# Optimization experiments

Hardware: AMD Instinct MI355X
Metric: run time of the kernel (lower is better)

## Reference

```python
import jax, jax.numpy as jnp
import numpy as np

B, T, F, H = 512, 1024, 64, 512  # batch, timesteps, n_features, hidden_dims


def _lstm_cell(x, h, c, W_ih, W_hh, b_ih, b_hh):
    # torch.nn.LSTMCell gate order: i, f, g, o
    g = x @ W_ih.T + b_ih + h @ W_hh.T + b_hh
    i, f, gg, o = jnp.split(g, 4, axis=-1)
    c_new = jax.nn.sigmoid(f) * c + jax.nn.sigmoid(i) * jnp.tanh(gg)
    h_new = jax.nn.sigmoid(o) * jnp.tanh(c_new)
    return h_new, c_new


def setup_inputs() -> dict:
    key = jax.random.key(0)
    ks = jax.random.split(key, 9)
    s1 = 1.0 / np.sqrt(H)  # torch LSTMCell init scale for lstm1
    s2 = 1.0 / np.sqrt(F)  # for lstm2 (hidden size = n_features)
    u = lambda k, shape, s: jax.random.uniform(k, shape, jnp.float32, -s, s)
    return {
        "data": jax.random.normal(ks[0], (B, T * F), jnp.float32),
        "W_ih1": u(ks[1], (4 * H, F), s1),
        "W_hh1": u(ks[2], (4 * H, H), s1),
        "b_ih1": u(ks[3], (4 * H,), s1),
        "b_hh1": u(ks[4], (4 * H,), s1),
        "W_ih2": u(ks[5], (4 * F, H), s2),
        "W_hh2": u(ks[6], (4 * F, F), s2),
        "b_ih2": u(ks[7], (4 * F,), s2),
        "b_hh2": u(ks[8], (4 * F,), s2),
        "future": 0,
    }


def reference(data, W_ih1, W_hh1, b_ih1, b_hh1, W_ih2, W_hh2, b_ih2, b_hh2, future):
    x = data.reshape(B, T, F).transpose(1, 0, 2)  # [T, B, F] for scan
    h1 = jnp.zeros((B, H), data.dtype)
    c1 = jnp.zeros((B, H), data.dtype)
    h2 = jnp.zeros((B, F), data.dtype)
    c2 = jnp.zeros((B, F), data.dtype)  # this is the 'output' in the torch code

    def step(carry, x_t):
        h1, c1, h2, c2 = carry
        h1, c1 = _lstm_cell(x_t, h1, c1, W_ih1, W_hh1, b_ih1, b_hh1)
        # NOTE: original feeds c_t (cell state of lstm1) into lstm2, and the
        # per-step 'output' is lstm2's CELL state c2 (h_t2, output = lstm2(...)).
        h2, c2 = _lstm_cell(c1, h2, c2, W_ih2, W_hh2, b_ih2, b_hh2)
        return (h1, c1, h2, c2), c2

    (h1, c1, h2, c2), outs = jax.lax.scan(step, (h1, c1, h2, c2), x)
    outputs = [outs]  # [T, B, F]
    out_t = c2
    for _ in range(int(future)):  # future is a Python int constant
        h1, c1 = _lstm_cell(out_t, h1, c1, W_ih1, W_hh1, b_ih1, b_hh1)
        h2, out_t = _lstm_cell(c1, h2, out_t, W_ih2, W_hh2, b_ih2, b_hh2)
        outputs.append(out_t[None])
    out = jnp.concatenate(outputs, axis=0).transpose(1, 0, 2)  # [B, T+future, F]
    return jnp.squeeze(out, axis=2) if out.shape[2] == 1 else out
```

## Files before the change

### kernel.cpp

```cpp
#include <hip/hip_runtime.h>

#define Bn   512
#define Tn   1024
#define Fn   64
#define Hn   512
#define NGRP 16
#define GMEM 9
#define NBLK (NGRP * GMEM)
#define TRIES (1L << 22)

typedef short bf16x8 __attribute__((ext_vector_type(8)));
typedef float f32x4  __attribute__((ext_vector_type(4)));

__device__ __forceinline__ short f2bf(float f) {
    union { float f; unsigned u; } v; v.f = f;
    unsigned r = (v.u + 0x7FFFu + ((v.u >> 16) & 1u)) >> 16;
    return (short)(unsigned short)r;
}
__device__ __forceinline__ float sigm(float x) { return 1.f / (1.f + __expf(-x)); }
__device__ __forceinline__ float tanh_(float x) { return 2.f / (1.f + __expf(-2.f * x)) - 1.f; }

__device__ __forceinline__ bf16x8 cvt8(const float* p) {
    const float4 v0 = *(const float4*)p;
    const float4 v1 = *(const float4*)(p + 4);
    bf16x8 a;
    a[0] = f2bf(v0.x); a[1] = f2bf(v0.y); a[2] = f2bf(v0.z); a[3] = f2bf(v0.w);
    a[4] = f2bf(v1.x); a[5] = f2bf(v1.y); a[6] = f2bf(v1.z); a[7] = f2bf(v1.w);
    return a;
}

__device__ __forceinline__ void ldx16(bf16x8& d, const short* p) {
    asm volatile("global_load_dwordx4 %0, %1, off sc0 sc1" : "=v"(d) : "v"(p));
}
__device__ __forceinline__ void stx16(short* p, bf16x8 v) {
    asm volatile("global_store_dwordx4 %0, %1, off sc0 sc1" :: "v"(p), "v"(v) : "memory");
}
#define VMWAIT(N) do { \
    asm volatile("s_waitcnt vmcnt(" #N ")" ::: "memory"); \
    __builtin_amdgcn_sched_barrier(0); } while (0)

__device__ __forceinline__ int aldi(const int* p) {
    return __hip_atomic_load(p, __ATOMIC_RELAXED, __HIP_MEMORY_SCOPE_AGENT);
}

__device__ __forceinline__ void flag_arrive(int* slot, int val) {
    asm volatile("s_waitcnt vmcnt(0)" ::: "memory");
    __builtin_amdgcn_sched_barrier(0);
    __syncthreads();
    if (threadIdx.x == 0)
        __hip_atomic_store(slot, val, __ATOMIC_RELEASE, __HIP_MEMORY_SCOPE_AGENT);
}
__device__ __forceinline__ void flag_wait(const int* flags, int tgtA, int tgtB) {
    const int lane = threadIdx.x & 63;
    const int tgt = (lane < 8) ? tgtA : tgtB;
    long spins = 0;
    for (;;) {
        bool ok = (lane >= GMEM) || (aldi(flags + lane) >= tgt);
        if (__all(ok)) break;
        if (++spins > TRIES) break;
        __builtin_amdgcn_s_sleep(1);
    }
    __atomic_signal_fence(__ATOMIC_ACQUIRE);
    __builtin_amdgcn_sched_barrier(0);
}

__global__ void prep_kernel(const float* __restrict__ Wih1, const float* __restrict__ Whh1,
                            const float* __restrict__ Wih2, const float* __restrict__ Whh2,
                            const float* __restrict__ bih1, const float* __restrict__ bhh1,
                            const float* __restrict__ bih2, const float* __restrict__ bhh2,
                            short* __restrict__ h1g, short* __restrict__ h2g,
                            short* __restrict__ w1f, short* __restrict__ w2f,
                            float* __restrict__ bs1, float* __restrict__ bs2,
                            int* __restrict__ bar) {
    const int i0 = blockIdx.x * blockDim.x + threadIdx.x;
    const int stride = gridDim.x * blockDim.x;
    for (int i = i0; i < 1024; i += stride) bar[i] = 0;
    for (int i = i0; i < 2 * Bn * Hn; i += stride) h1g[i] = 0;
    for (int i = i0; i < 2 * Bn * Fn; i += stride) h2g[i] = 0;
    for (int i = i0; i < 2048 * 576; i += stride) {
        int kk = i & 31, n = (i >> 5) & 15, ct = (i >> 9) & 3;
        int r = i >> 11; int kb = r % 18; int ut = r / 18;
        int gcol = ct * 512 + ut * 16 + n;
        int k = kb * 32 + kk;
        float v = (k < 64) ? Wih1[gcol * 64 + k] : Whh1[gcol * 512 + (k - 64)];
        w1f[i] = f2bf(v);
    }
    for (int i = i0; i < 256 * 576; i += stride) {
        int kk = i & 31, n = (i >> 5) & 15, ct = (i >> 9) & 3;
        int r = i >> 11; int kb = r % 18; int ut4 = r / 18;
        int gcol = ct * 64 + ut4 * 16 + n;
        int k = kb * 32 + kk;
        float v = (k < 512) ? Wih2[gcol * 512 + k] : Whh2[gcol * 64 + (k - 512)];
        w2f[i] = f2bf(v);
    }
    for (int i = i0; i < 2048; i += stride) bs1[i] = bih1[i] + bhh1[i];
    for (int i = i0; i < 256;  i += stride) bs2[i] = bih2[i] + bhh2[i];
}

__global__ __launch_bounds__(256, 1) void lstm_kernel(
    const float* __restrict__ data,
    const short* __restrict__ w1f, const float* __restrict__ bs1,
    const short* __restrict__ w2f, const float* __restrict__ bs2,
    short* __restrict__ h1g, short* __restrict__ c1g,
    float* __restrict__ out, int* __restrict__ bar) {
    extern __shared__ short smem[];
    const int tid = threadIdx.x;
    const int lane = tid & 63, wv = tid >> 6;
    const int n = lane & 15, q = lane >> 4;
    const int wvc = wv;
    const int bid = blockIdx.x;
    const int rt = bid / GMEM, role = bid % GMEM;
    const f32x4 Z4 = {0.f, 0.f, 0.f, 0.f};
    const int rowbase = rt * 32;
    int* grp = bar + rt * 32;
    short* tile0 = smem + 16384;
    short* tile1 = smem + 18432;
    const int r0 = rowbase + n, r1 = rowbase + 16 + n;
    const int lr0 = n, lr1 = n + 16, sw = n & 7;

    if (role < 8) {
        const int ut = role * 4 + wvc;
        const int ucol = ut * 16 + n;
        const float bi_ = bs1[ucol], bf_ = bs1[512 + ucol], bg_ = bs1[1024 + ucol], bo_ = bs1[1536 + ucol];
        const short* wbase = w1f + ut * 36864 + n * 32 + q * 8;

        bf16x8 wr[16][4];
#pragma unroll
        for (int kb = 0; kb < 16; ++kb)
#pragma unroll
            for (int g = 0; g < 4; ++g)
                wr[kb][g] = *(const bf16x8*)(wbase + ((kb + 2) * 4 + g) * 512);

        f32x4 c1f[2]; c1f[0] = Z4; c1f[1] = Z4;

        for (int t = 0; t < Tn; ++t) {
            const short* h1r = h1g + (t & 1) * (Bn * Hn);
            short* h1w = h1g + ((t + 1) & 1) * (Bn * Hn);
            short* c1w = c1g + (t & 1) * (Bn * Hn);
            f32x4 acc[2][4];
#pragma unroll
            for (int a = 0; a < 2; ++a)
#pragma unroll
                for (int g = 0; g < 4; ++g) acc[a][g] = Z4;

            const float* x0 = data + (size_t)r0 * 65536 + t * 64;
            const float* x1 = data + (size_t)r1 * 65536 + t * 64;
#pragma unroll
            for (int kb = 0; kb < 2; ++kb) {
                const bf16x8 a0 = cvt8(x0 + kb * 32 + q * 8);
                const bf16x8 a1 = cvt8(x1 + kb * 32 + q * 8);
#pragma unroll
                for (int g = 0; g < 4; ++g) {
                    const bf16x8 b = *(const bf16x8*)(wbase + (kb * 4 + g) * 512);
                    acc[0][g] = __builtin_amdgcn_mfma_f32_16x16x32_bf16(a0, b, acc[0][g], 0, 0, 0);
                    acc[1][g] = __builtin_amdgcn_mfma_f32_16x16x32_bf16(a1, b, acc[1][g], 0, 0, 0);
                }
            }

            flag_wait(grp, t, t - 1);

            const short* gsrc = h1r + (size_t)rt * 16384;
            bf16x8 st[8];
            __builtin_amdgcn_sched_barrier(0);
#pragma unroll
            for (int i = 0; i < 8; ++i) ldx16(st[i], gsrc + (i * 256 + tid) * 8);
            VMWAIT(4);
#pragma unroll
            for (int i = 0; i < 4; ++i) {
                const int c = i * 256 + tid; const int row = c >> 6, col = c & 63;
                *(bf16x8*)&smem[row * 512 + ((col ^ (row & 7)) * 8)] = st[i];
            }
            VMWAIT(0);
#pragma unroll
            for (int i = 4; i < 8; ++i) {
                const int c = i * 256 + tid; const int row = c >> 6, col = c & 63;
                *(bf16x8*)&smem[row * 512 + ((col ^ (row & 7)) * 8)] = st[i];
            }
            __syncthreads();

#pragma unroll
            for (int kb = 0; kb < 16; ++kb) {
                const bf16x8 a0 = *(const bf16x8*)&smem[lr0 * 512 + (((kb * 4 + q) ^ sw) * 8)];
                const bf16x8 a1 = *(const bf16x8*)&smem[lr1 * 512 + (((kb * 4 + q) ^ sw) * 8)];
#pragma unroll
                for (int g = 0; g < 4; ++g) {
                    acc[0][g] = __builtin_amdgcn_mfma_f32_16x16x32_bf16(a0, wr[kb][g], acc[0][g], 0, 0, 0);
                    acc[1][g] = __builtin_amdgcn_mfma_f32_16x16x32_bf16(a1, wr[kb][g], acc[1][g], 0, 0, 0);
                }
            }

#pragma unroll
            for (int rt16 = 0; rt16 < 2; ++rt16) {
#pragma unroll
                for (int r = 0; r < 4; ++r) {
                    const float xi = acc[rt16][0][r] + bi_;
                    const float xf = acc[rt16][1][r] + bf_;
                    const float xg = acc[rt16][2][r] + bg_;
                    const float xo = acc[rt16][3][r] + bo_;
                    const float ii = sigm(xi), ff = sigm(xf), gg = tanh_(xg), oo = sigm(xo);
                    const float c = ff * c1f[rt16][r] + ii * gg;
                    c1f[rt16][r] = c;
                    const float h = oo * tanh_(c);
                    const int lr = rt16 * 16 + q * 4 + r;
                    const int lu = wvc * 16 + n;
                    tile0[lr * 64 + lu] = f2bf(h);
                    tile1[lr * 64 + lu] = f2bf(c);
                }
            }
            __syncthreads();
            {
                const int row = tid >> 3, part = tid & 7;
                const bf16x8 hv = *(const bf16x8*)&tile0[row * 64 + part * 8];
                const bf16x8 cv = *(const bf16x8*)&tile1[row * 64 + part * 8];
                short* gdst = h1w + (size_t)(rowbase + row) * 512 + role * 64 + part * 8;
                short* gdc  = c1w + (size_t)(rowbase + row) * 512 + role * 64 + part * 8;
                stx16(gdst, hv);
                stx16(gdc, cv);
            }
            flag_arrive(grp + role, t + 1);
        }
    } else {
        const int ut4 = wvc;
        const int ucol = ut4 * 16 + n;
        const float bi_ = bs2[ucol], bf_ = bs2[64 + ucol], bg_ = bs2[128 + ucol], bo_ = bs2[192 + ucol];
        const short* wbase = w2f + ut4 * 36864 + n * 32 + q * 8;

        bf16x8 wr[16][4];
#pragma unroll
        for (int kb = 0; kb < 16; ++kb)
#pragma unroll
            for (int g = 0; g < 4; ++g)
                wr[kb][g] = *(const bf16x8*)(wbase + (kb * 4 + g) * 512);
        bf16x8 wh[2][4];
#pragma unroll
        for (int kb2 = 0; kb2 < 2; ++kb2)
#pragma unroll
            for (int g = 0; g < 4; ++g)
                wh[kb2][g] = *(const bf16x8*)(wbase + ((16 + kb2) * 4 + g) * 512);

        for (int i = tid; i < 2048; i += 256) { tile0[i] = 0; tile1[i] = 0; }
        __syncthreads();

        f32x4 c2f[2]; c2f[0] = Z4; c2f[1] = Z4;

        for (int t = 0; t < Tn; ++t) {
            flag_wait(grp, t + 1, t);
            const short* c1r = c1g + (t & 1) * (Bn * Hn);
            const short* h2rd = (t & 1) ? tile1 : tile0;
            short* h2wr = (t & 1) ? tile0 : tile1;
            f32x4 acc[2][4];
#pragma unroll
            for (int a = 0; a < 2; ++a)
#pragma unroll
                for (int g = 0; g < 4; ++g) acc[a][g] = Z4;

            const short* gsrc = c1r + (size_t)rt * 16384;
            bf16x8 st[8];
            __builtin_amdgcn_sched_barrier(0);
#pragma unroll
            for (int i = 0; i < 8; ++i) ldx16(st[i], gsrc + (i * 256 + tid) * 8);
            VMWAIT(4);
#pragma unroll
            for (int i = 0; i < 4; ++i) {
                const int c = i * 256 + tid; const int row = c >> 6, col = c & 63;
                *(bf16x8*)&smem[row * 512 + ((col ^ (row & 7)) * 8)] = st[i];
            }
            VMWAIT(0);
#pragma unroll
            for (int i = 4; i < 8; ++i) {
                const int c = i * 256 + tid; const int row = c >> 6, col = c & 63;
                *(bf16x8*)&smem[row * 512 + ((col ^ (row & 7)) * 8)] = st[i];
            }
            __syncthreads();

#pragma unroll
            for (int kb = 0; kb < 16; ++kb) {
                const bf16x8 a0 = *(const bf16x8*)&smem[lr0 * 512 + (((kb * 4 + q) ^ sw) * 8)];
                const bf16x8 a1 = *(const bf16x8*)&smem[lr1 * 512 + (((kb * 4 + q) ^ sw) * 8)];
#pragma unroll
                for (int g = 0; g < 4; ++g) {
                    acc[0][g] = __builtin_amdgcn_mfma_f32_16x16x32_bf16(a0, wr[kb][g], acc[0][g], 0, 0, 0);
                    acc[1][g] = __builtin_amdgcn_mfma_f32_16x16x32_bf16(a1, wr[kb][g], acc[1][g], 0, 0, 0);
                }
            }
#pragma unroll
            for (int kb2 = 0; kb2 < 2; ++kb2) {
                const bf16x8 a0 = *(const bf16x8*)&h2rd[lr0 * 64 + (((kb2 * 4 + q) ^ sw) * 8)];
                const bf16x8 a1 = *(const bf16x8*)&h2rd[lr1 * 64 + (((kb2 * 4 + q) ^ sw) * 8)];
#pragma unroll
                for (int g = 0; g < 4; ++g) {
                    acc[0][g] = __builtin_amdgcn_mfma_f32_16x16x32_bf16(a0, wh[kb2][g], acc[0][g], 0, 0, 0);
                    acc[1][g] = __builtin_amdgcn_mfma_f32_16x16x32_bf16(a1, wh[kb2][g], acc[1][g], 0, 0, 0);
                }
            }

#pragma unroll
            for (int rt16 = 0; rt16 < 2; ++rt16) {
#pragma unroll
                for (int r = 0; r < 4; ++r) {
                    const float xi = acc[rt16][0][r] + bi_;
                    const float xf = acc[rt16][1][r] + bf_;
                    const float xg = acc[rt16][2][r] + bg_;
                    const float xo = acc[rt16][3][r] + bo_;
                    const float ii = sigm(xi), ff = sigm(xf), gg = tanh_(xg), oo = sigm(xo);
                    const float c = ff * c2f[rt16][r] + ii * gg;
                    c2f[rt16][r] = c;
                    const float h = oo * tanh_(c);
                    const int lr = rt16 * 16 + q * 4 + r;
                    const int lu = wvc * 16 + n;
                    out[(size_t)(rowbase + lr) * 65536 + (size_t)t * 64 + ucol] = c;
                    h2wr[lr * 64 + (((lu >> 3) ^ (lr & 7)) * 8) + (lu & 7)] = f2bf(h);
                }
            }
            flag_arrive(grp + 8, t + 1);
        }
    }
}

extern "C" void kernel_launch(void* const* d_in, const int* in_sizes, int n_in,
                              void* d_out, int out_size, void* d_ws, size_t ws_size,
                              hipStream_t stream) {
    const float* data = (const float*)d_in[0];
    const float* Wih1 = (const float*)d_in[1];
    const float* Whh1 = (const float*)d_in[2];
    const float* bih1 = (const float*)d_in[3];
    const float* bhh1 = (const float*)d_in[4];
    const float* Wih2 = (const float*)d_in[5];
    const float* Whh2 = (const float*)d_in[6];
    const float* bih2 = (const float*)d_in[7];
    const float* bhh2 = (const float*)d_in[8];
    float* out = (float*)d_out;

    char* w = (char*)d_ws;
    short* h1g = (short*)(w + 0);
    short* c1g = (short*)(w + 1048576);
    short* h2g = (short*)(w + 2097152);
    short* w2f = (short*)(w + 2228224);
    short* w1f = (short*)(w + 2523136);
    float* bs1 = (float*)(w + 4882432);
    float* bs2 = (float*)(w + 4890624);
    int* bar  = (int*)(w + 4891648);

    hipLaunchKernelGGL(prep_kernel, dim3(1024), dim3(256), 0, stream,
                       Wih1, Whh1, Wih2, Whh2, bih1, bhh1, bih2, bhh2,
                       h1g, h2g, w1f, w2f, bs1, bs2, bar);

    hipLaunchKernelGGL(lstm_kernel, dim3(NBLK), dim3(256), 40960, stream,
                       data, w1f, bs1, w2f, bs2, h1g, c1g, out, bar);
}
```

Before: 7.511 ms.

## Triple-buffer c1 handoff, reuse own h1 slice locally, pad LDS rows

The c1 exchange buffer becomes triple-buffered, so layer-1 blocks only wait for layer-2 to be two steps behind instead of one, which loosens coupling between the two stages. Each layer-1 block now loads only the seven foreign 64-column slices of h1 from global memory and takes its own slice from the local LDS tile written in the previous step, saving one global load per thread per step. LDS row strides are padded (516 and 68) and the tile writes are swizzled to reduce bank conflicts. The h1 store flag is raised before the c1 store, and a final arrive is added after the loop. This adds more workspace and more complex synchronisation logic.

```diff
diff --git a/kernel.cpp b/kernel.cpp
--- a/kernel.cpp
+++ b/kernel.cpp
@@ -8,6 +8,8 @@
 #define GMEM 9
 #define NBLK (NGRP * GMEM)
 #define TRIES (1L << 22)
+#define SLD  516
+#define TLD  68
 
 typedef short bf16x8 __attribute__((ext_vector_type(8)));
 typedef float f32x4  __attribute__((ext_vector_type(4)));
@@ -68,7 +70,7 @@
                             const float* __restrict__ Wih2, const float* __restrict__ Whh2,
                             const float* __restrict__ bih1, const float* __restrict__ bhh1,
                             const float* __restrict__ bih2, const float* __restrict__ bhh2,
-                            short* __restrict__ h1g, short* __restrict__ h2g,
+                            short* __restrict__ h1g, short* __restrict__ c1g,
                             short* __restrict__ w1f, short* __restrict__ w2f,
                             float* __restrict__ bs1, float* __restrict__ bs2,
                             int* __restrict__ bar) {
@@ -76,7 +78,7 @@
     const int stride = gridDim.x * blockDim.x;
     for (int i = i0; i < 1024; i += stride) bar[i] = 0;
     for (int i = i0; i < 2 * Bn * Hn; i += stride) h1g[i] = 0;
-    for (int i = i0; i < 2 * Bn * Fn; i += stride) h2g[i] = 0;
+    for (int i = i0; i < 3 * Bn * Hn; i += stride) c1g[i] = 0;
     for (int i = i0; i < 2048 * 576; i += stride) {
         int kk = i & 31, n = (i >> 5) & 15, ct = (i >> 9) & 3;
         int r = i >> 11; int kb = r % 18; int ut = r / 18;
@@ -113,10 +115,11 @@
     const f32x4 Z4 = {0.f, 0.f, 0.f, 0.f};
     const int rowbase = rt * 32;
     int* grp = bar + rt * 32;
-    short* tile0 = smem + 16384;
-    short* tile1 = smem + 18432;
+    short* tile0 = smem + 32 * SLD;
+    short* tile1 = tile0 + 32 * TLD;
     const int r0 = rowbase + n, r1 = rowbase + 16 + n;
     const int lr0 = n, lr1 = n + 16, sw = n & 7;
+    const int srow = tid >> 3, sd8 = tid & 7;
 
     if (role < 8) {
         const int ut = role * 4 + wvc;
@@ -131,12 +134,15 @@
             for (int g = 0; g < 4; ++g)
                 wr[kb][g] = *(const bf16x8*)(wbase + ((kb + 2) * 4 + g) * 512);
 
+        for (int i = tid; i < 32 * TLD; i += 256) tile0[i] = 0;
+        __syncthreads();
+
         f32x4 c1f[2]; c1f[0] = Z4; c1f[1] = Z4;
 
         for (int t = 0; t < Tn; ++t) {
             const short* h1r = h1g + (t & 1) * (Bn * Hn);
             short* h1w = h1g + ((t + 1) & 1) * (Bn * Hn);
-            short* c1w = c1g + (t & 1) * (Bn * Hn);
+            short* c1w = c1g + (t % 3) * (Bn * Hn);
             f32x4 acc[2][4];
 #pragma unroll
             for (int a = 0; a < 2; ++a)
@@ -156,32 +162,47 @@
                     acc[1][g] = __builtin_amdgcn_mfma_f32_16x16x32_bf16(a1, b, acc[1][g], 0, 0, 0);
                 }
             }
-
-            flag_wait(grp, t, t - 1);
-
-            const short* gsrc = h1r + (size_t)rt * 16384;
-            bf16x8 st[8];
+            bf16x8 aOwn[2][2];
+#pragma unroll
+            for (int kl = 0; kl < 2; ++kl) {
+                aOwn[kl][0] = *(const bf16x8*)&tile0[lr0 * TLD + ((((kl * 4 + q)) ^ sw) * 8)];
+                aOwn[kl][1] = *(const bf16x8*)&tile0[lr1 * TLD + ((((kl * 4 + q)) ^ sw) * 8)];
+            }
+
+            flag_wait(grp, t, t - 2);
+
+            const short* gsrc = h1r + (size_t)rowbase * 512;
+            bf16x8 st[7];
             __builtin_amdgcn_sched_barrier(0);
 #pragma unroll
-            for (int i = 0; i < 8; ++i) ldx16(st[i], gsrc + (i * 256 + tid) * 8);
-            VMWAIT(4);
+            for (int i = 0; i < 7; ++i) {
+                const int p = (role + 1 + i) & 7;
+                ldx16(st[i], gsrc + srow * 512 + p * 64 + sd8 * 8);
+            }
+            VMWAIT(3);
 #pragma unroll
             for (int i = 0; i < 4; ++i) {
-                const int c = i * 256 + tid; const int row = c >> 6, col = c & 63;
-                *(bf16x8*)&smem[row * 512 + ((col ^ (row & 7)) * 8)] = st[i];
+                const int p = (role + 1 + i) & 7;
+                *(bf16x8*)&smem[srow * SLD + ((p * 8 + (sd8 ^ (srow & 7))) * 8)] = st[i];
             }
             VMWAIT(0);
 #pragma unroll
-            for (int i = 4; i < 8; ++i) {
-                const int c = i * 256 + tid; const int row = c >> 6, col = c & 63;
-                *(bf16x8*)&smem[row * 512 + ((col ^ (row & 7)) * 8)] = st[i];
+            for (int i = 4; i < 7; ++i) {
+                const int p = (role + 1 + i) & 7;
+                *(bf16x8*)&smem[srow * SLD + ((p * 8 + (sd8 ^ (srow & 7))) * 8)] = st[i];
             }
             __syncthreads();
 
 #pragma unroll
             for (int kb = 0; kb < 16; ++kb) {
-                const bf16x8 a0 = *(const bf16x8*)&smem[lr0 * 512 + (((kb * 4 + q) ^ sw) * 8)];
-                const bf16x8 a1 = *(const bf16x8*)&smem[lr1 * 512 + (((kb * 4 + q) ^ sw) * 8)];
+                bf16x8 a0, a1;
+                if ((kb >> 1) == role) {
+                    a0 = aOwn[kb & 1][0];
+                    a1 = aOwn[kb & 1][1];
+                } else {
+                    a0 = *(const bf16x8*)&smem[lr0 * SLD + (((kb * 4 + q) ^ sw) * 8)];
+                    a1 = *(const bf16x8*)&smem[lr1 * SLD + (((kb * 4 + q) ^ sw) * 8)];
+                }
 #pragma unroll
                 for (int g = 0; g < 4; ++g) {
                     acc[0][g] = __builtin_amdgcn_mfma_f32_16x16x32_bf16(a0, wr[kb][g], acc[0][g], 0, 0, 0);
@@ -203,22 +224,25 @@
                     const float h = oo * tanh_(c);
                     const int lr = rt16 * 16 + q * 4 + r;
                     const int lu = wvc * 16 + n;
-                    tile0[lr * 64 + lu] = f2bf(h);
-                    tile1[lr * 64 + lu] = f2bf(c);
+                    const int slot = ((lu >> 3) ^ (lr & 7)) * 8 + (lu & 7);
+                    tile0[lr * TLD + slot] = f2bf(h);
+                    tile1[lr * TLD + slot] = f2bf(c);
                 }
             }
             __syncthreads();
             {
                 const int row = tid >> 3, part = tid & 7;
-                const bf16x8 hv = *(const bf16x8*)&tile0[row * 64 + part * 8];
-                const bf16x8 cv = *(const bf16x8*)&tile1[row * 64 + part * 8];
+                const int slot = (part ^ (row & 7)) * 8;
+                const bf16x8 hv = *(const bf16x8*)&tile0[row * TLD + slot];
+                const bf16x8 cv = *(const bf16x8*)&tile1[row * TLD + slot];
                 short* gdst = h1w + (size_t)(rowbase + row) * 512 + role * 64 + part * 8;
                 short* gdc  = c1w + (size_t)(rowbase + row) * 512 + role * 64 + part * 8;
                 stx16(gdst, hv);
+                flag_arrive(grp + role, t + 1);
                 stx16(gdc, cv);
             }
-            flag_arrive(grp + role, t + 1);
         }
+        flag_arrive(grp + role, Tn + 1);
     } else {
         const int ut4 = wvc;
         const int ucol = ut4 * 16 + n;
@@ -238,14 +262,14 @@
             for (int g = 0; g < 4; ++g)
                 wh[kb2][g] = *(const bf16x8*)(wbase + ((16 + kb2) * 4 + g) * 512);
 
-        for (int i = tid; i < 2048; i += 256) { tile0[i] = 0; tile1[i] = 0; }
+        for (int i = tid; i < 64 * TLD; i += 256) tile0[i] = 0;
         __syncthreads();
 
         f32x4 c2f[2]; c2f[0] = Z4; c2f[1] = Z4;
 
         for (int t = 0; t < Tn; ++t) {
-            flag_wait(grp, t + 1, t);
-            const short* c1r = c1g + (t & 1) * (Bn * Hn);
+            flag_wait(grp, t + 2, t);
+            const short* c1r = c1g + (t % 3) * (Bn * Hn);
             const short* h2rd = (t & 1) ? tile1 : tile0;
             short* h2wr = (t & 1) ? tile0 : tile1;
             f32x4 acc[2][4];
@@ -254,7 +278,7 @@
 #pragma unroll
                 for (int g = 0; g < 4; ++g) acc[a][g] = Z4;
 
-            const short* gsrc = c1r + (size_t)rt * 16384;
+            const short* gsrc = c1r + (size_t)rowbase * 512;
             bf16x8 st[8];
             __builtin_amdgcn_sched_barrier(0);
 #pragma unroll
@@ -262,21 +286,21 @@
             VMWAIT(4);
 #pragma unroll
             for (int i = 0; i < 4; ++i) {
-                const int c = i * 256 + tid; const int row = c >> 6, col = c & 63;
-                *(bf16x8*)&smem[row * 512 + ((col ^ (row & 7)) * 8)] = st[i];
+                const int row = i * 4 + wv; const int col = lane;
+                *(bf16x8*)&smem[row * SLD + ((col >> 3) * 8 + ((col & 7) ^ (row & 7))) * 8] = st[i];
             }
             VMWAIT(0);
 #pragma unroll
             for (int i = 4; i < 8; ++i) {
-                const int c = i * 256 + tid; const int row = c >> 6, col = c & 63;
-                *(bf16x8*)&smem[row * 512 + ((col ^ (row & 7)) * 8)] = st[i];
+                const int row = i * 4 + wv; const int col = lane;
+                *(bf16x8*)&smem[row * SLD + ((col >> 3) * 8 + ((col & 7) ^ (row & 7))) * 8] = st[i];
             }
             __syncthreads();
 
 #pragma unroll
             for (int kb = 0; kb < 16; ++kb) {
-                const bf16x8 a0 = *(const bf16x8*)&smem[lr0 * 512 + (((kb * 4 + q) ^ sw) * 8)];
-                const bf16x8 a1 = *(const bf16x8*)&smem[lr1 * 512 + (((kb * 4 + q) ^ sw) * 8)];
+                const bf16x8 a0 = *(const bf16x8*)&smem[lr0 * SLD + (((kb * 4 + q) ^ sw) * 8)];
+                const bf16x8 a1 = *(const bf16x8*)&smem[lr1 * SLD + (((kb * 4 + q) ^ sw) * 8)];
 #pragma unroll
                 for (int g = 0; g < 4; ++g) {
                     acc[0][g] = __builtin_amdgcn_mfma_f32_16x16x32_bf16(a0, wr[kb][g], acc[0][g], 0, 0, 0);
@@ -285,8 +309,8 @@
             }
 #pragma unroll
             for (int kb2 = 0; kb2 < 2; ++kb2) {
-                const bf16x8 a0 = *(const bf16x8*)&h2rd[lr0 * 64 + (((kb2 * 4 + q) ^ sw) * 8)];
-                const bf16x8 a1 = *(const bf16x8*)&h2rd[lr1 * 64 + (((kb2 * 4 + q) ^ sw) * 8)];
+                const bf16x8 a0 = *(const bf16x8*)&h2rd[lr0 * TLD + (((kb2 * 4 + q) ^ sw) * 8)];
+                const bf16x8 a1 = *(const bf16x8*)&h2rd[lr1 * TLD + (((kb2 * 4 + q) ^ sw) * 8)];
 #pragma unroll
                 for (int g = 0; g < 4; ++g) {
                     acc[0][g] = __builtin_amdgcn_mfma_f32_16x16x32_bf16(a0, wh[kb2][g], acc[0][g], 0, 0, 0);
@@ -309,7 +333,7 @@
                     const int lr = rt16 * 16 + q * 4 + r;
                     const int lu = wvc * 16 + n;
                     out[(size_t)(rowbase + lr) * 65536 + (size_t)t * 64 + ucol] = c;
-                    h2wr[lr * 64 + (((lu >> 3) ^ (lr & 7)) * 8) + (lu & 7)] = f2bf(h);
+                    h2wr[lr * TLD + ((lu >> 3) ^ (lr & 7)) * 8 + (lu & 7)] = f2bf(h);
                 }
             }
             flag_arrive(grp + 8, t + 1);
@@ -334,17 +358,17 @@
     char* w = (char*)d_ws;
     short* h1g = (short*)(w + 0);
     short* c1g = (short*)(w + 1048576);
-    short* h2g = (short*)(w + 2097152);
-    short* w2f = (short*)(w + 2228224);
-    short* w1f = (short*)(w + 2523136);
-    float* bs1 = (float*)(w + 4882432);
-    float* bs2 = (float*)(w + 4890624);
-    int* bar  = (int*)(w + 4891648);
+    short* w2f = (short*)(w + 2621440);
+    short* w1f = (short*)(w + 2916352);
+    float* bs1 = (float*)(w + 5275648);
+    float* bs2 = (float*)(w + 5283840);
+    int* bar  = (int*)(w + 5284864);
 
     hipLaunchKernelGGL(prep_kernel, dim3(1024), dim3(256), 0, stream,
                        Wih1, Whh1, Wih2, Whh2, bih1, bhh1, bih2, bhh2,
-                       h1g, h2g, w1f, w2f, bs1, bs2, bar);
-
-    hipLaunchKernelGGL(lstm_kernel, dim3(NBLK), dim3(256), 40960, stream,
+                       h1g, c1g, w1f, w2f, bs1, bs2, bar);
+
+    const int lds_bytes = (32 * SLD + 64 * TLD) * 2;
+    hipLaunchKernelGGL(lstm_kernel, dim3(NBLK), dim3(256), lds_bytes, stream,
                        data, w1f, bs1, w2f, bs2, h1g, c1g, out, bar);
 }
```

Result: slower. 10.04 ms (+33.6%).
